# Kernel optimization log

Measured on AMD Instinct MI355X. Metric: run time of the kernel, lower is better.

## Reference

```python
import jax, jax.numpy as jnp
import numpy as np


def setup_inputs() -> dict:
    key = jax.random.key(0)
    k1, k2 = jax.random.split(key)
    B, C, D = 8192, 8192, 256
    x = jax.random.normal(k1, (B, D), dtype=jnp.float32)
    y = jax.random.normal(k2, (C, D), dtype=jnp.float32)
    gamma = jnp.ones((), dtype=jnp.float32)
    return {"x": x, "y": y, "gamma": gamma}


def reference(x, y, gamma):
    # RBF kernel: exp(-gamma * ||x_i - y_j||^2), shape (B, C).
    # avoiding the O(B*C*D) broadcast-diff intermediate of the naive form.
    x2 = jnp.sum(x * x, axis=-1)          # (B,)
    y2 = jnp.sum(y * y, axis=-1)          # (C,)
    xy = jnp.einsum('bd,cd->bc', x, y)    # (B, C) GEMM
    sq_dist = x2[:, None] + y2[None, :] - 2.0 * xy
    sq_dist = jnp.maximum(sq_dist, 0.0)   # guard tiny negatives from cancellation
    return jnp.exp(-gamma * sq_dist)
```

## Files before the change

### kernel.cpp

```cpp
#include <hip/hip_runtime.h>
#include <hip/hip_bf16.h>

typedef __bf16 bf16_t;
typedef __attribute__((ext_vector_type(8))) __bf16 bf16x8;
typedef __attribute__((ext_vector_type(4))) __bf16 bf16x4;
typedef __attribute__((ext_vector_type(4))) float floatx4;

#define NB 8192
#define NC 8192
#define ND 256
#define BM 128
#define BN 128
#define BK 32

typedef __attribute__((address_space(3))) void lds_void_t;
typedef __attribute__((address_space(1))) void gl_void_t;

__global__ __launch_bounds__(256) void prep_kernel(
    const float* __restrict__ x, const float* __restrict__ y,
    bf16_t* __restrict__ xb, bf16_t* __restrict__ yb,
    float* __restrict__ x2, float* __restrict__ y2)
{
    int t    = threadIdx.x;
    int wave = t >> 6;
    int lane = t & 63;
    int row  = blockIdx.x * 4 + wave;

    const float* src;
    bf16_t* dst;
    float* nrm;
    int r;
    if (row < NB) { src = x; dst = xb; nrm = x2; r = row; }
    else          { src = y; dst = yb; nrm = y2; r = row - NB; }

    float4 v = ((const float4*)(src + (size_t)r * ND))[lane];
    float ss = v.x * v.x + v.y * v.y + v.z * v.z + v.w * v.w;

    bf16x4 o;
    o.x = (__bf16)v.x; o.y = (__bf16)v.y; o.z = (__bf16)v.z; o.w = (__bf16)v.w;
    ((bf16x4*)(dst + (size_t)r * ND))[lane] = o;

    #pragma unroll
    for (int off = 32; off >= 1; off >>= 1)
        ss += __shfl_xor(ss, off, 64);
    if (lane == 0) nrm[r] = ss;
}

__global__ __launch_bounds__(256) void rbf_gemm_kernel(
    const bf16_t* __restrict__ xb, const bf16_t* __restrict__ yb,
    const float* __restrict__ x2, const float* __restrict__ y2,
    const float* __restrict__ gamma_p, float* __restrict__ out)
{
    __shared__ bf16_t lA[BM * BK];
    __shared__ bf16_t lB[BN * BK];

    const int t    = threadIdx.x;
    const int lane = t & 63;
    const int wave = t >> 6;
    const int wm   = wave >> 1;
    const int wn   = wave & 1;
    const int quad = lane >> 4;
    const int l15  = lane & 15;

    const int bm = blockIdx.x * BM;
    const int bn = blockIdx.y * BN;

    const float gamma = *gamma_p;

    floatx4 acc[4][4];
    #pragma unroll
    for (int i = 0; i < 4; ++i)
        #pragma unroll
        for (int j = 0; j < 4; ++j)
            acc[i][j] = (floatx4){0.f, 0.f, 0.f, 0.f};

    const char* gA = (const char*)xb + (size_t)bm * (ND * 2);
    const char* gB = (const char*)yb + (size_t)bn * (ND * 2);

    for (int kt = 0; kt < ND / BK; ++kt) {
        __syncthreads();
        #pragma unroll
        for (int c = 0; c < 2; ++c) {
            const int li  = c * 256 + t;
            const int row = li >> 2;
            const int kb  = (li & 3) * 16;
            const size_t goff = (size_t)row * (ND * 2) + kt * (BK * 2) + kb;
            __builtin_amdgcn_global_load_lds(
                (gl_void_t*)(gA + goff),
                (lds_void_t*)((char*)lA + (size_t)li * 16), 16, 0, 0);
            __builtin_amdgcn_global_load_lds(
                (gl_void_t*)(gB + goff),
                (lds_void_t*)((char*)lB + (size_t)li * 16), 16, 0, 0);
        }
        __syncthreads();

        bf16x8 af[4], bfr[4];
        #pragma unroll
        for (int i = 0; i < 4; ++i) {
            const int ar = wm * 64 + i * 16 + l15;
            af[i]  = *(const bf16x8*)((const char*)lA + ar * (BK * 2) + quad * 16);
            const int br = wn * 64 + i * 16 + l15;
            bfr[i] = *(const bf16x8*)((const char*)lB + br * (BK * 2) + quad * 16);
        }
        #pragma unroll
        for (int i = 0; i < 4; ++i)
            #pragma unroll
            for (int j = 0; j < 4; ++j)
                acc[i][j] = __builtin_amdgcn_mfma_f32_16x16x32_bf16(
                    af[i], bfr[j], acc[i][j], 0, 0, 0);
    }

    #pragma unroll
    for (int i = 0; i < 4; ++i) {
        const int grow0 = bm + wm * 64 + i * 16 + quad * 4;
        float xn[4];
        #pragma unroll
        for (int r = 0; r < 4; ++r) xn[r] = x2[grow0 + r];
        #pragma unroll
        for (int j = 0; j < 4; ++j) {
            const int gcol = bn + wn * 64 + j * 16 + l15;
            const float yn = y2[gcol];
            #pragma unroll
            for (int r = 0; r < 4; ++r) {
                float sq = xn[r] + yn - 2.0f * acc[i][j][r];
                sq = fmaxf(sq, 0.0f);
                out[(size_t)(grow0 + r) * NC + gcol] = __expf(-gamma * sq);
            }
        }
    }
}

extern "C" void kernel_launch(void* const* d_in, const int* in_sizes, int n_in,
                              void* d_out, int out_size, void* d_ws, size_t ws_size,
                              hipStream_t stream) {
    const float* x = (const float*)d_in[0];
    const float* y = (const float*)d_in[1];
    const float* gamma = (const float*)d_in[2];
    float* out = (float*)d_out;

    bf16_t* xb = (bf16_t*)d_ws;
    bf16_t* yb = xb + (size_t)NB * ND;
    float*  x2 = (float*)(yb + (size_t)NC * ND);
    float*  y2 = x2 + NB;

    prep_kernel<<<dim3((NB + NC) / 4), dim3(256), 0, stream>>>(x, y, xb, yb, x2, y2);
    rbf_gemm_kernel<<<dim3(NB / BM, NC / BN), dim3(256), 0, stream>>>(
        xb, yb, x2, y2, gamma, out);
}
```

Before: 297.8 us.

## Double K tile with XOR-swizzled LDS and fold gamma into exp2 epilogue

Raises the K tile from 32 to 64, so the K loop runs 4 times instead of 8 and there are half as many barrier pairs. LDS writes and reads now use an XOR swizzle by row to cut bank conflicts on the wider rows. Gamma times log2(e) is folded into the precomputed norms, and the epilogue becomes one FMA, a min and exp2. Launch bounds now request 4 blocks per SIMD. The larger tiles double LDS use and may raise register pressure, which could limit occupancy.

```diff
diff --git a/kernel.cpp b/kernel.cpp
--- a/kernel.cpp
+++ b/kernel.cpp
@@ -11,15 +11,17 @@
 #define ND 256
 #define BM 128
 #define BN 128
-#define BK 32
+#define BK 64
+#define LOG2E 1.44269504088896340736f
 
 typedef __attribute__((address_space(3))) void lds_void_t;
 typedef __attribute__((address_space(1))) void gl_void_t;
 
 __global__ __launch_bounds__(256) void prep_kernel(
     const float* __restrict__ x, const float* __restrict__ y,
+    const float* __restrict__ gamma_p,
     bf16_t* __restrict__ xb, bf16_t* __restrict__ yb,
-    float* __restrict__ x2, float* __restrict__ y2)
+    float* __restrict__ x2s, float* __restrict__ y2s)
 {
     int t    = threadIdx.x;
     int wave = t >> 6;
@@ -30,8 +32,8 @@
     bf16_t* dst;
     float* nrm;
     int r;
-    if (row < NB) { src = x; dst = xb; nrm = x2; r = row; }
-    else          { src = y; dst = yb; nrm = y2; r = row - NB; }
+    if (row < NB) { src = x; dst = xb; nrm = x2s; r = row; }
+    else          { src = y; dst = yb; nrm = y2s; r = row - NB; }
 
     float4 v = ((const float4*)(src + (size_t)r * ND))[lane];
     float ss = v.x * v.x + v.y * v.y + v.z * v.z + v.w * v.w;
@@ -43,12 +45,12 @@
     #pragma unroll
     for (int off = 32; off >= 1; off >>= 1)
         ss += __shfl_xor(ss, off, 64);
-    if (lane == 0) nrm[r] = ss;
+    if (lane == 0) nrm[r] = ss * (LOG2E * gamma_p[0]);
 }
 
-__global__ __launch_bounds__(256) void rbf_gemm_kernel(
+__global__ __launch_bounds__(256, 4) void rbf_gemm_kernel(
     const bf16_t* __restrict__ xb, const bf16_t* __restrict__ yb,
-    const float* __restrict__ x2, const float* __restrict__ y2,
+    const float* __restrict__ x2s, const float* __restrict__ y2s,
     const float* __restrict__ gamma_p, float* __restrict__ out)
 {
     __shared__ bf16_t lA[BM * BK];
@@ -65,7 +67,7 @@
     const int bm = blockIdx.x * BM;
     const int bn = blockIdx.y * BN;
 
-    const float gamma = *gamma_p;
+    const float A2 = 2.0f * LOG2E * gamma_p[0];
 
     floatx4 acc[4][4];
     #pragma unroll
@@ -80,11 +82,12 @@
     for (int kt = 0; kt < ND / BK; ++kt) {
         __syncthreads();
         #pragma unroll
-        for (int c = 0; c < 2; ++c) {
+        for (int c = 0; c < 4; ++c) {
             const int li  = c * 256 + t;
-            const int row = li >> 2;
-            const int kb  = (li & 3) * 16;
-            const size_t goff = (size_t)row * (ND * 2) + kt * (BK * 2) + kb;
+            const int row = li >> 3;
+            const int kb  = (li & 7) * 16;
+            const int kbs = kb ^ ((row & 7) << 4);
+            const size_t goff = (size_t)row * (ND * 2) + kt * (BK * 2) + kbs;
             __builtin_amdgcn_global_load_lds(
                 (gl_void_t*)(gA + goff),
                 (lds_void_t*)((char*)lA + (size_t)li * 16), 16, 0, 0);
@@ -94,20 +97,25 @@
         }
         __syncthreads();
 
-        bf16x8 af[4], bfr[4];
         #pragma unroll
-        for (int i = 0; i < 4; ++i) {
-            const int ar = wm * 64 + i * 16 + l15;
-            af[i]  = *(const bf16x8*)((const char*)lA + ar * (BK * 2) + quad * 16);
-            const int br = wn * 64 + i * 16 + l15;
-            bfr[i] = *(const bf16x8*)((const char*)lB + br * (BK * 2) + quad * 16);
+        for (int kk = 0; kk < 2; ++kk) {
+            bf16x8 af[4], bfr[4];
+            const int swz = ((l15 & 7) << 4);
+            const int off = (kk * 64 + quad * 16) ^ swz;
+            #pragma unroll
+            for (int i = 0; i < 4; ++i) {
+                const int ar = wm * 64 + i * 16 + l15;
+                af[i]  = *(const bf16x8*)((const char*)lA + ar * (BK * 2) + off);
+                const int br = wn * 64 + i * 16 + l15;
+                bfr[i] = *(const bf16x8*)((const char*)lB + br * (BK * 2) + off);
+            }
+            #pragma unroll
+            for (int i = 0; i < 4; ++i)
+                #pragma unroll
+                for (int j = 0; j < 4; ++j)
+                    acc[i][j] = __builtin_amdgcn_mfma_f32_16x16x32_bf16(
+                        af[i], bfr[j], acc[i][j], 0, 0, 0);
         }
-        #pragma unroll
-        for (int i = 0; i < 4; ++i)
-            #pragma unroll
-            for (int j = 0; j < 4; ++j)
-                acc[i][j] = __builtin_amdgcn_mfma_f32_16x16x32_bf16(
-                    af[i], bfr[j], acc[i][j], 0, 0, 0);
     }
 
     #pragma unroll
@@ -115,16 +123,16 @@
         const int grow0 = bm + wm * 64 + i * 16 + quad * 4;
         float xn[4];
         #pragma unroll
-        for (int r = 0; r < 4; ++r) xn[r] = x2[grow0 + r];
+        for (int r = 0; r < 4; ++r) xn[r] = x2s[grow0 + r];
         #pragma unroll
         for (int j = 0; j < 4; ++j) {
             const int gcol = bn + wn * 64 + j * 16 + l15;
-            const float yn = y2[gcol];
+            const float yn = y2s[gcol];
             #pragma unroll
             for (int r = 0; r < 4; ++r) {
-                float sq = xn[r] + yn - 2.0f * acc[i][j][r];
-                sq = fmaxf(sq, 0.0f);
-                out[(size_t)(grow0 + r) * NC + gcol] = __expf(-gamma * sq);
+                float t2 = fmaf(A2, acc[i][j][r], -(xn[r] + yn));
+                t2 = fminf(t2, 0.0f);
+                out[(size_t)(grow0 + r) * NC + gcol] = exp2f(t2);
             }
         }
     }
@@ -140,10 +148,11 @@
 
     bf16_t* xb = (bf16_t*)d_ws;
     bf16_t* yb = xb + (size_t)NB * ND;
-    float*  x2 = (float*)(yb + (size_t)NC * ND);
-    float*  y2 = x2 + NB;
+    float*  x2s = (float*)(yb + (size_t)NC * ND);
+    float*  y2s = x2s + NB;
 
-    prep_kernel<<<dim3((NB + NC) / 4), dim3(256), 0, stream>>>(x, y, xb, yb, x2, y2);
+    prep_kernel<<<dim3((NB + NC) / 4), dim3(256), 0, stream>>>(
+        x, y, gamma, xb, yb, x2s, y2s);
     rbf_gemm_kernel<<<dim3(NB / BM, NC / BN), dim3(256), 0, stream>>>(
-        xb, yb, x2, y2, gamma, out);
+        xb, yb, x2s, y2s, gamma, out);
 }
```

After: 334.4 us. 12.3% more time.
